# Performance work log

Hardware: AMD Instinct MI355X
Metric: run time of the kernel (lower is better)

## Reference

```python
import math
import jax, jax.numpy as jnp
import numpy as np

E = 1024
H = 16
DH = E // H
R = 8
ALPHA = 16
LORA_S = ALPHA / R

def build_slopes(h):
    start = 2 ** (-2 ** (-(math.log2(h) - 3)))
    return jnp.asarray([start * start ** i for i in range(h)], dtype=jnp.float32)

def setup_inputs() -> dict:
    key = jax.random.key(0)
    ks = jax.random.split(key, 12)
    B, T = 2, 2048
    x = jax.random.normal(ks[0], (B, T, E), dtype=jnp.float32)
    # nn.Linear weights: [out_f, in_f]; LoRA A: [out_f, r], B: [r, in_f]
    def lin(k):
        return jax.random.normal(k, (E, E), dtype=jnp.float32) / math.sqrt(E)
    inp = {
        "x": x,
        "Wq": lin(ks[1]), "Aq": jax.random.normal(ks[2], (E, R)) * 0.01, "Bq": jax.random.normal(ks[3], (R, E)) * 0.01,
        "Wk": lin(ks[4]), "Ak": jax.random.normal(ks[5], (E, R)) * 0.01, "Bk": jax.random.normal(ks[6], (R, E)) * 0.01,
        "Wv": lin(ks[7]), "Av": jax.random.normal(ks[8], (E, R)) * 0.01, "Bv": jax.random.normal(ks[9], (R, E)) * 0.01,
        "Wp": lin(ks[10]),
    }
    return inp

def _lora(x, W, A, Bm):
    # x @ W.T + (x @ B.T) @ A.T * s
    return x @ W.T + ((x @ Bm.T) @ A.T) * LORA_S

def reference(x, Wq, Aq, Bq, Wk, Ak, Bk, Wv, Av, Bv, Wp):
    B, T, _ = x.shape
    slopes = build_slopes(H)  # [H]
    q = _lora(x, Wq, Aq, Bq).reshape(B, T, H, DH).transpose(0, 2, 1, 3)  # [B,H,T,dh]
    k = _lora(x, Wk, Ak, Bk).reshape(B, T, H, DH).transpose(0, 2, 1, 3)
    v = _lora(x, Wv, Av, Bv).reshape(B, T, H, DH).transpose(0, 2, 1, 3)
    s = jnp.einsum("bhqd,bhkd->bhqk", q, k) / math.sqrt(DH)
    i = jnp.arange(T, dtype=jnp.float32)[:, None]
    j = jnp.arange(T, dtype=jnp.float32)[None, :]
    alibi = slopes[:, None, None] * (i - j)  # [H,T,T]
    mask = jnp.triu(jnp.full((T, T), -jnp.inf, dtype=jnp.float32), 1)
    s = s + alibi[None] + mask
    p = jax.nn.softmax(s, axis=-1)
    o = jnp.einsum("bhqk,bhkd->bhqd", p, v).transpose(0, 2, 1, 3).reshape(B, T, E)
    return o @ Wp.T
```

## Files before the change

### kernel.cpp

```cpp
#include <hip/hip_runtime.h>

typedef unsigned short u16;
typedef unsigned int   u32;
typedef __bf16 bf16_t;
typedef bf16_t bf16x8 __attribute__((ext_vector_type(8)));
typedef bf16_t bf16x2v __attribute__((ext_vector_type(2)));
typedef float  f32x4  __attribute__((ext_vector_type(4)));

#define E_DIM 1024
#define T_DIM 2048
#define H_NUM 16
#define DH 64
#define BT 4096
#define Y_LD 2048

__device__ __forceinline__ u16 f2bf(float f) {
  u32 u = __builtin_bit_cast(u32, f);
  u32 r = (u + 0x7fffu + ((u >> 16) & 1u)) >> 16;
  return (u16)r;
}
__device__ __forceinline__ float bf2f(u16 v) {
  u32 u = ((u32)v) << 16;
  return __builtin_bit_cast(float, u);
}

__device__ __forceinline__ float fexp2(float x) {
#if __has_builtin(__builtin_amdgcn_exp2f)
  return __builtin_amdgcn_exp2f(x);
#else
  return exp2f(x);
#endif
}

__device__ __forceinline__ int swz(int r, int c) {
  return r * 64 + (c ^ ((r & 7) << 3));
}

__device__ __forceinline__ void store_val(float* p, float v) { *p = v; }
__device__ __forceinline__ void store_val(u16* p, float v)   { *p = f2bf(v); }

typedef __attribute__((address_space(3))) unsigned int as3_u32;
typedef const __attribute__((address_space(1))) unsigned int as1_u32;

__device__ __forceinline__ void async16(const u16* g, u16* l) {
  __builtin_amdgcn_global_load_lds((as1_u32*)g, (as3_u32*)l, 16, 0, 0);
}

__device__ __forceinline__ void waitvm0_barrier() {
  asm volatile("s_waitcnt vmcnt(0)" ::: "memory");
  __builtin_amdgcn_s_barrier();
  __builtin_amdgcn_sched_barrier(0);
}

__device__ __forceinline__ u32 pack2(float a, float b) {
  bf16x2v v;
  v[0] = (bf16_t)a;
  v[1] = (bf16_t)b;
  return __builtin_bit_cast(u32, v);
}

__device__ __forceinline__ void plswap(u32& a, u32& b) {
#if __has_builtin(__builtin_amdgcn_permlane32_swap)
  typedef u32 u32x2 __attribute__((ext_vector_type(2)));
  u32x2 r = __builtin_amdgcn_permlane32_swap(a, b, false, false);
  a = r[0];
  b = r[1];
#else
  asm volatile("v_permlane32_swap_b32 %0, %1" : "+v"(a), "+v"(b));
#endif
}

__device__ __forceinline__ void redist_pair(u32 A, u32 B, bool odd, u32& wj, u32& wj2) {
  plswap(A, B);
  u32 sA = __builtin_amdgcn_ds_swizzle(A, 0x401F);
  u32 sB = __builtin_amdgcn_ds_swizzle(B, 0x401F);
  wj  = odd ? sB : A;
  wj2 = odd ? B : sA;
}

__global__ __launch_bounds__(256) void k_prep(
    const float* __restrict__ x,
    const float* __restrict__ W0, const float* __restrict__ A0, const float* __restrict__ B0,
    const float* __restrict__ W1, const float* __restrict__ A1, const float* __restrict__ B1,
    const float* __restrict__ W2, const float* __restrict__ A2, const float* __restrict__ B2,
    const float* __restrict__ Wp,
    u16* __restrict__ xb, u16* __restrict__ Weff, u16* __restrict__ Wpb, float s0) {
  const int blk = blockIdx.x;
  const int tid = threadIdx.x;
  if (blk < 4096) {
    int i = (blk * 256 + tid) * 4;
    float4 v = *reinterpret_cast<const float4*>(x + i);
    u32 lo = (u32)f2bf(v.x) | ((u32)f2bf(v.y) << 16);
    u32 hi = (u32)f2bf(v.z) | ((u32)f2bf(v.w) << 16);
    *reinterpret_cast<uint2*>(xb + i) = make_uint2(lo, hi);
  } else if (blk < 7168) {
    int e4 = (blk - 4096) * 256 + tid;
    int m = e4 >> 18;
    int e = (e4 & 262143) * 4;
    const float* W  = (m == 0) ? W0 : (m == 1) ? W1 : W2;
    const float* A  = (m == 0) ? A0 : (m == 1) ? A1 : A2;
    const float* Bm = (m == 0) ? B0 : (m == 1) ? B1 : B2;
    const float sc  = (m == 0) ? s0 : 1.0f;
    int o = e >> 10, i = e & 1023;
    float4 wv = *reinterpret_cast<const float4*>(W + e);
    float acc[4] = {wv.x, wv.y, wv.z, wv.w};
#pragma unroll
    for (int r = 0; r < 8; ++r) {
      float a2 = 2.0f * A[o * 8 + r];
      float4 bv = *reinterpret_cast<const float4*>(Bm + r * 1024 + i);
      acc[0] += a2 * bv.x; acc[1] += a2 * bv.y; acc[2] += a2 * bv.z; acc[3] += a2 * bv.w;
    }
    u32 lo = (u32)f2bf(acc[0] * sc) | ((u32)f2bf(acc[1] * sc) << 16);
    u32 hi = (u32)f2bf(acc[2] * sc) | ((u32)f2bf(acc[3] * sc) << 16);
    *reinterpret_cast<uint2*>(Weff + (size_t)m * 1048576 + e) = make_uint2(lo, hi);
  } else {
    int i = ((blk - 7168) * 256 + tid) * 4;
    float4 v = *reinterpret_cast<const float4*>(Wp + i);
    u32 lo = (u32)f2bf(v.x) | ((u32)f2bf(v.y) << 16);
    u32 hi = (u32)f2bf(v.z) | ((u32)f2bf(v.w) << 16);
    *reinterpret_cast<uint2*>(Wpb + i) = make_uint2(lo, hi);
  }
}

template <typename OUT_T, bool QKV>
__global__ __launch_bounds__(512) void k_gemm2(
    const u16* __restrict__ A, const u16* __restrict__ B,
    OUT_T* __restrict__ C, u16* __restrict__ Vt, int K, int ldc) {
  __shared__ __align__(16) u16 As[2][8192];
  __shared__ __align__(16) u16 Bs[2][8192];
  const int tid  = threadIdx.x;
  const int lane = tid & 63;
  const int wave = tid >> 6;
  const int wr = wave >> 2;
  const int wc = wave & 3;
  const int m0 = blockIdx.y * 128;
  const int n0 = blockIdx.x * 128;
  const int lr = lane & 15;
  const int lk = (lane >> 4) * 8;
  const bool vmode = QKV && (n0 >= 2048);

  f32x4 acc[4][2] = {};

  auto stageg = [&](int bufi, int t) {
#pragma unroll
    for (int p = 0; p < 2; ++p) {
      const int off = (p * 8 + wave) * 512;
      const int e = off + lane * 8;
      const int r = e >> 6, c = e & 63;
      const int cs = c ^ ((r & 7) << 3);
      async16(&A[(size_t)(m0 + r) * K + t * 64 + cs], &As[bufi][off]);
      async16(&B[(size_t)(n0 + r) * K + t * 64 + cs], &Bs[bufi][off]);
    }
  };

  const int nt = K >> 6;
  stageg(0, 0);
  waitvm0_barrier();
  int buf = 0;

  for (int t = 0; t < nt; ++t) {
    if (t + 1 < nt) stageg(buf ^ 1, t + 1);
    __builtin_amdgcn_s_setprio(1);
#pragma unroll
    for (int kk = 0; kk < 2; ++kk) {
      bf16x8 af[4], bfr[2];
#pragma unroll
      for (int mi = 0; mi < 4; ++mi)
        af[mi] = *reinterpret_cast<const bf16x8*>(&As[buf][swz(wr * 64 + mi * 16 + lr, kk * 32 + lk)]);
#pragma unroll
      for (int ni = 0; ni < 2; ++ni)
        bfr[ni] = *reinterpret_cast<const bf16x8*>(&Bs[buf][swz(wc * 32 + ni * 16 + lr, kk * 32 + lk)]);
      if (vmode) {
#pragma unroll
        for (int mi = 0; mi < 4; ++mi)
#pragma unroll
          for (int ni = 0; ni < 2; ++ni)
            acc[mi][ni] = __builtin_amdgcn_mfma_f32_16x16x32_bf16(bfr[ni], af[mi], acc[mi][ni], 0, 0, 0);
      } else {
#pragma unroll
        for (int mi = 0; mi < 4; ++mi)
#pragma unroll
          for (int ni = 0; ni < 2; ++ni)
            acc[mi][ni] = __builtin_amdgcn_mfma_f32_16x16x32_bf16(af[mi], bfr[ni], acc[mi][ni], 0, 0, 0);
      }
    }
    __builtin_amdgcn_s_setprio(0);
    waitvm0_barrier();
    buf ^= 1;
  }

  const int rg = (lane >> 4) * 4;
  if (vmode) {
#pragma unroll
    for (int mi = 0; mi < 4; ++mi)
#pragma unroll
      for (int ni = 0; ni < 2; ++ni)
#pragma unroll
        for (int q = 0; q < 4; ++q) {
          int o = n0 - 2048 + wc * 32 + ni * 16 + rg + q;
          int h = o >> 6, d = o & 63;
          int rowm = m0 + wr * 64 + mi * 16 + lr;
          int b = rowm >> 11, t = rowm & 2047;
          Vt[(size_t)(((b << 4) + h) * 64 + d) * 2048 + t] = f2bf(acc[mi][ni][q]);
        }
  } else {
#pragma unroll
    for (int mi = 0; mi < 4; ++mi)
#pragma unroll
      for (int ni = 0; ni < 2; ++ni)
#pragma unroll
        for (int q = 0; q < 4; ++q) {
          int row = m0 + wr * 64 + mi * 16 + rg + q;
          int col = n0 + wc * 32 + ni * 16 + lr;
          store_val(&C[(size_t)row * ldc + col], acc[mi][ni][q]);
        }
  }
}

__global__ __launch_bounds__(256) void k_attn8(
    const u16* __restrict__ Y, const u16* __restrict__ Vt, u16* __restrict__ Og,
    u16* __restrict__ Oa, u16* __restrict__ Ob,
    float* __restrict__ la, float* __restrict__ lb) {
  __shared__ __align__(16) u16 Ks[2][4096];
  __shared__ __align__(16) u16 Vs[2][4096];

  const int tid = threadIdx.x;
  const int lane = tid & 63;
  const int wave = tid >> 6;
  const int lr = lane & 15;
  const int lg = lane >> 4;
  const int lk = lg * 8;
  const bool odd = (lane & 16) != 0;

  const int orig = blockIdx.x;
  const int bh = orig & 31;
  const int c  = orig >> 5;
  const int qt = (c < 16) ? (16 + c) : (47 - c);
  const int ks = (c >= 16 && c < 32) ? 16 : 0;
  int ke       = (c < 16) ? 15 : qt;
  const int b = bh >> 4, h = bh & 15;

  const float LOG2E = 1.4426950408889634f;
  const float slope2 = exp2f(-0.5f * (float)(h + 1)) * LOG2E;

  const int Th = min(32, (int)(150.0f / slope2) / 64 + 1);
  ke = min(ke, Th - 1);

  if (ks > ke) {
    const int base = b * 1024 + (qt * 64 - 1024);
#pragma unroll
    for (int p = 0; p < 2; ++p) {
      int idx = p * 256 + tid;
      int rr = idx >> 3, cc8 = (idx & 7) * 8;
      uint4 z = {0, 0, 0, 0};
      *reinterpret_cast<uint4*>(&Ob[(size_t)(base + rr) * E_DIM + h * DH + cc8]) = z;
    }
    if (tid < 64) lb[bh * 1024 + (qt * 64 - 1024) + tid] = 0.f;
    return;
  }

  const u16* Kb = Y + (size_t)b * T_DIM * Y_LD + 1024 + h * DH;
  const u16* Vb = Vt + (size_t)bh * DH * T_DIM;

  bf16x8 qf[2];
  {
    const int qrow = qt * 64 + wave * 16 + lr;
#pragma unroll
    for (int kk = 0; kk < 2; ++kk)
      qf[kk] = *reinterpret_cast<const bf16x8*>(
          &Y[(size_t)(b * T_DIM + qrow) * Y_LD + h * DH + kk * 32 + lk]);
  }

  float nkb[16];
#pragma unroll
  for (int ni = 0; ni < 4; ++ni)
#pragma unroll
    for (int r = 0; r < 4; ++r)
      nkb[ni * 4 + r] = -slope2 * (float)(ni * 16 + lg * 4 + r) - 12.0f;

  bf16x8 ones;
#pragma unroll
  for (int jj = 0; jj < 8; ++jj) ones[jj] = (bf16_t)1.0f;

  f32x4 oacc[4] = {};
  f32x4 lacc = {};

  auto stage = [&](int bufi, int kt) {
    const int kv0 = kt * 64;
#pragma unroll
    for (int q = 0; q < 2; ++q) {
      const int off = (q * 4 + wave) * 512;
      const int e = off + lane * 8;
      const int r = e >> 6, cc = e & 63;
      const int cs = cc ^ ((r & 7) << 3);
      async16(Kb + (size_t)(kv0 + r) * Y_LD + cs, &Ks[bufi][off]);
      async16(Vb + (size_t)r * T_DIM + kv0 + cs, &Vs[bufi][off]);
    }
  };

  auto step = [&](int kt, int buf, bool DIAG) {
    f32x4 s[4] = {};
    __builtin_amdgcn_s_setprio(1);
#pragma unroll
    for (int kk = 0; kk < 2; ++kk)
#pragma unroll
      for (int ni = 0; ni < 4; ++ni) {
        bf16x8 kf = *reinterpret_cast<const bf16x8*>(&Ks[buf][swz(ni * 16 + lr, kk * 32 + lk)]);
        s[ni] = __builtin_amdgcn_mfma_f32_16x16x32_bf16(kf, qf[kk], s[ni], 0, 0, 0);
      }
    __builtin_amdgcn_s_setprio(0);
    const float ck = -slope2 * (float)(kt * 64);
    u32 pk[4][2];
#pragma unroll
    for (int ni = 0; ni < 4; ++ni) {
      float p[4];
#pragma unroll
      for (int r = 0; r < 4; ++r) {
        float sc = s[ni][r] + nkb[ni * 4 + r] + ck;
        if (DIAG && (ni * 16 + lg * 4 + r) > (wave * 16 + lr)) sc = -INFINITY;
        p[r] = fexp2(sc);
      }
      pk[ni][0] = pack2(p[0], p[1]);
      pk[ni][1] = pack2(p[2], p[3]);
    }
    uint4 PW[2];
#pragma unroll
    for (int kk = 0; kk < 2; ++kk) {
      redist_pair(pk[2 * kk][0], pk[2 * kk + 1][0], odd, PW[kk].x, PW[kk].z);
      redist_pair(pk[2 * kk][1], pk[2 * kk + 1][1], odd, PW[kk].y, PW[kk].w);
    }
    __builtin_amdgcn_s_setprio(1);
#pragma unroll
    for (int kk = 0; kk < 2; ++kk) {
      bf16x8 ph = __builtin_bit_cast(bf16x8, PW[kk]);
      lacc = __builtin_amdgcn_mfma_f32_16x16x32_bf16(ph, ones, lacc, 0, 0, 0);
#pragma unroll
      for (int f = 0; f < 4; ++f) {
        bf16x8 vf = *reinterpret_cast<const bf16x8*>(&Vs[buf][swz(f * 16 + lr, kk * 32 + lk)]);
        oacc[f] = __builtin_amdgcn_mfma_f32_16x16x32_bf16(ph, vf, oacc[f], 0, 0, 0);
      }
    }
    __builtin_amdgcn_s_setprio(0);
  };

  stage(0, ks);
  waitvm0_barrier();
  int buf = 0;
  for (int kt = ks; kt <= ke; ++kt) {
    if (kt < ke) stage(buf ^ 1, kt + 1);
    step(kt, buf, kt == qt);
    waitvm0_barrier();
    buf ^= 1;
  }

  if (c >= 32) {
    float linv[4];
#pragma unroll
    for (int r = 0; r < 4; ++r) linv[r] = 1.0f / lacc[r];
#pragma unroll
    for (int f = 0; f < 4; ++f)
#pragma unroll
      for (int r = 0; r < 4; ++r) {
        int q = qt * 64 + wave * 16 + lg * 4 + r;
        Og[(size_t)(b * T_DIM + q) * E_DIM + h * DH + f * 16 + lr] =
            f2bf(oacc[f][r] * linv[r]);
      }
  } else {
    u16* Op   = (c < 16) ? Oa : Ob;
    float* lp = (c < 16) ? la : lb;
#pragma unroll
    for (int f = 0; f < 4; ++f)
#pragma unroll
      for (int r = 0; r < 4; ++r) {
        int q = qt * 64 + wave * 16 + lg * 4 + r;
        Op[(size_t)(b * 1024 + (q - 1024)) * E_DIM + h * DH + f * 16 + lr] =
            f2bf(oacc[f][r]);
      }
    if (lr == 0) {
#pragma unroll
      for (int r = 0; r < 4; ++r) {
        int q = qt * 64 + wave * 16 + lg * 4 + r;
        lp[bh * 1024 + (q - 1024)] = lacc[r];
      }
    }
  }
}

__global__ __launch_bounds__(256) void k_merge(
    const u16* __restrict__ Oa, const u16* __restrict__ Ob,
    const float* __restrict__ la, const float* __restrict__ lb,
    u16* __restrict__ Og) {
  int idx = blockIdx.x * 256 + threadIdx.x;
  int row = idx >> 8;
  int cg  = (idx & 255) * 4;
  int b = row >> 10, tl = row & 1023;
  int h = cg >> 6;
  size_t po = (size_t)row * E_DIM + cg;
  uint2 ua = *reinterpret_cast<const uint2*>(Oa + po);
  uint2 ub = *reinterpret_cast<const uint2*>(Ob + po);
  float l = la[((b << 4) + h) * 1024 + tl] + lb[((b << 4) + h) * 1024 + tl];
  float inv = 1.0f / l;
  const u16* pa = reinterpret_cast<const u16*>(&ua);
  const u16* pb = reinterpret_cast<const u16*>(&ub);
  u16 o[4];
#pragma unroll
  for (int j = 0; j < 4; ++j)
    o[j] = f2bf((bf2f(pa[j]) + bf2f(pb[j])) * inv);
  *reinterpret_cast<uint2*>(Og + (size_t)(b * T_DIM + 1024 + tl) * E_DIM + cg) =
      *reinterpret_cast<const uint2*>(o);
}

extern "C" void kernel_launch(void* const* d_in, const int* in_sizes, int n_in,
                              void* d_out, int out_size, void* d_ws, size_t ws_size,
                              hipStream_t stream) {
  const float* x  = (const float*)d_in[0];
  const float* Wq = (const float*)d_in[1];
  const float* Aq = (const float*)d_in[2];
  const float* Bq = (const float*)d_in[3];
  const float* Wk = (const float*)d_in[4];
  const float* Ak = (const float*)d_in[5];
  const float* Bk = (const float*)d_in[6];
  const float* Wv = (const float*)d_in[7];
  const float* Av = (const float*)d_in[8];
  const float* Bv = (const float*)d_in[9];
  const float* Wp = (const float*)d_in[10];
  float* out = (float*)d_out;

  char* ws = (char*)d_ws;
  const size_t MB = 1048576;
  u16* xb   = (u16*)(ws);
  u16* Oa   = (u16*)(ws);
  u16* Ob   = (u16*)(ws + 4 * MB);
  u16* Weff = (u16*)(ws + 8 * MB);
  float* la = (float*)(ws + 8 * MB);
  float* lb = (float*)(ws + 8 * MB + 131072);
  u16* Yq   = (u16*)(ws + 14 * MB);
  u16* VtB  = (u16*)(ws + 30 * MB);
  u16* Wpb  = (u16*)(ws + 38 * MB);
  u16* Og   = (u16*)(ws + 40 * MB);

  const float ISQ2 = 0.125f * 1.4426950408889634f;

  k_prep<<<8192, 256, 0, stream>>>(x, Wq, Aq, Bq, Wk, Ak, Bk, Wv, Av, Bv, Wp,
                                   xb, Weff, Wpb, ISQ2);
  {
    dim3 grid(24, 32);
    k_gemm2<u16, true><<<grid, 512, 0, stream>>>(xb, Weff, Yq, VtB, E_DIM, Y_LD);
  }
  k_attn8<<<1536, 256, 0, stream>>>(Yq, VtB, Og, Oa, Ob, la, lb);
  k_merge<<<2048, 256, 0, stream>>>(Oa, Ob, la, lb, Og);
  {
    dim3 grid(8, 32);
    k_gemm2<float, false><<<grid, 512, 0, stream>>>(Og, Wpb, out, nullptr, E_DIM, E_DIM);
  }
}
```

Before: 107.6 us.

## Fuse split-attention merge into output projection and tighten ALiBi key cutoff

Removes the standalone merge kernel. The output projection GEMM now combines the two partial attention outputs, normalises them by the summed row sums and packs to bf16 while loading its A tile for the upper half of the sequence, which avoids a write and re-read of the merged activations. The attention grid is remapped so heads are scheduled from the highest index down with batch interleaved, for better load balance. The ALiBi distance cutoff is lowered from 150 to 64 log2 units so more far-away key tiles are skipped. The fused A-path uses synchronous global loads and register stores instead of async LDS copies, which may weaken load/compute overlap in the projection GEMM.

```diff
diff --git a/kernel.cpp b/kernel.cpp
--- a/kernel.cpp
+++ b/kernel.cpp
@@ -36,9 +36,6 @@
   return r * 64 + (c ^ ((r & 7) << 3));
 }
 
-__device__ __forceinline__ void store_val(float* p, float v) { *p = v; }
-__device__ __forceinline__ void store_val(u16* p, float v)   { *p = f2bf(v); }
-
 typedef __attribute__((address_space(3))) unsigned int as3_u32;
 typedef const __attribute__((address_space(1))) unsigned int as1_u32;
 
@@ -48,6 +45,12 @@
 
 __device__ __forceinline__ void waitvm0_barrier() {
   asm volatile("s_waitcnt vmcnt(0)" ::: "memory");
+  __builtin_amdgcn_s_barrier();
+  __builtin_amdgcn_sched_barrier(0);
+}
+
+__device__ __forceinline__ void waitall_barrier() {
+  asm volatile("s_waitcnt vmcnt(0) lgkmcnt(0)" ::: "memory");
   __builtin_amdgcn_s_barrier();
   __builtin_amdgcn_sched_barrier(0);
 }
@@ -122,10 +125,9 @@
   }
 }
 
-template <typename OUT_T, bool QKV>
 __global__ __launch_bounds__(512) void k_gemm2(
     const u16* __restrict__ A, const u16* __restrict__ B,
-    OUT_T* __restrict__ C, u16* __restrict__ Vt, int K, int ldc) {
+    u16* __restrict__ C, u16* __restrict__ Vt, int K, int ldc) {
   __shared__ __align__(16) u16 As[2][8192];
   __shared__ __align__(16) u16 Bs[2][8192];
   const int tid  = threadIdx.x;
@@ -137,7 +139,7 @@
   const int n0 = blockIdx.x * 128;
   const int lr = lane & 15;
   const int lk = (lane >> 4) * 8;
-  const bool vmode = QKV && (n0 >= 2048);
+  const bool vmode = (n0 >= 2048);
 
   f32x4 acc[4][2] = {};
 
@@ -212,9 +214,98 @@
         for (int q = 0; q < 4; ++q) {
           int row = m0 + wr * 64 + mi * 16 + rg + q;
           int col = n0 + wc * 32 + ni * 16 + lr;
-          store_val(&C[(size_t)row * ldc + col], acc[mi][ni][q]);
+          C[(size_t)row * ldc + col] = f2bf(acc[mi][ni][q]);
         }
   }
+}
+
+__global__ __launch_bounds__(512) void k_projm(
+    const u16* __restrict__ Og, const u16* __restrict__ Oa, const u16* __restrict__ Ob,
+    const float* __restrict__ la, const float* __restrict__ lb,
+    const u16* __restrict__ B, float* __restrict__ C) {
+  __shared__ __align__(16) u16 As[2][8192];
+  __shared__ __align__(16) u16 Bs[2][8192];
+  const int tid  = threadIdx.x;
+  const int lane = tid & 63;
+  const int wave = tid >> 6;
+  const int wr = wave >> 2, wc = wave & 3;
+  const int m0 = blockIdx.y * 128;
+  const int n0 = blockIdx.x * 128;
+  const int lr = lane & 15;
+  const int lk = (lane >> 4) * 8;
+  const bool upper = (m0 & 2047) >= 1024;
+  const int K = 1024;
+
+  f32x4 acc[4][2] = {};
+
+  auto stageg = [&](int bufi, int t) {
+#pragma unroll
+    for (int p = 0; p < 2; ++p) {
+      const int off = (p * 8 + wave) * 512;
+      const int e = off + lane * 8;
+      const int r = e >> 6, c = e & 63;
+      const int cs = c ^ ((r & 7) << 3);
+      async16(&B[(size_t)(n0 + r) * K + t * 64 + cs], &Bs[bufi][off]);
+      if (!upper) {
+        async16(&Og[(size_t)(m0 + r) * K + t * 64 + cs], &As[bufi][off]);
+      } else {
+        const int rowg = m0 + r;
+        const int bb = rowg >> 11, tl = (rowg & 2047) - 1024;
+        const int li = (bb * 16 + t) * 1024 + tl;
+        const float inv = 1.0f / (la[li] + lb[li]);
+        size_t po = (size_t)(bb * 1024 + tl) * 1024 + t * 64 + cs;
+        uint4 va = *reinterpret_cast<const uint4*>(Oa + po);
+        uint4 vb = *reinterpret_cast<const uint4*>(Ob + po);
+        const u16* pa = reinterpret_cast<const u16*>(&va);
+        const u16* pb = reinterpret_cast<const u16*>(&vb);
+        u16 o[8];
+#pragma unroll
+        for (int j = 0; j < 8; ++j) o[j] = f2bf((bf2f(pa[j]) + bf2f(pb[j])) * inv);
+        *reinterpret_cast<uint4*>(&As[bufi][off + lane * 8]) =
+            *reinterpret_cast<const uint4*>(o);
+      }
+    }
+  };
+
+  const int nt = K >> 6;
+  stageg(0, 0);
+  waitall_barrier();
+  int buf = 0;
+
+  for (int t = 0; t < nt; ++t) {
+    if (t + 1 < nt) stageg(buf ^ 1, t + 1);
+    __builtin_amdgcn_s_setprio(1);
+#pragma unroll
+    for (int kk = 0; kk < 2; ++kk) {
+      bf16x8 af[4], bfr[2];
+#pragma unroll
+      for (int mi = 0; mi < 4; ++mi)
+        af[mi] = *reinterpret_cast<const bf16x8*>(&As[buf][swz(wr * 64 + mi * 16 + lr, kk * 32 + lk)]);
+#pragma unroll
+      for (int ni = 0; ni < 2; ++ni)
+        bfr[ni] = *reinterpret_cast<const bf16x8*>(&Bs[buf][swz(wc * 32 + ni * 16 + lr, kk * 32 + lk)]);
+#pragma unroll
+      for (int mi = 0; mi < 4; ++mi)
+#pragma unroll
+        for (int ni = 0; ni < 2; ++ni)
+          acc[mi][ni] = __builtin_amdgcn_mfma_f32_16x16x32_bf16(af[mi], bfr[ni], acc[mi][ni], 0, 0, 0);
+    }
+    __builtin_amdgcn_s_setprio(0);
+    waitall_barrier();
+    buf ^= 1;
+  }
+
+  const int rg = (lane >> 4) * 4;
+#pragma unroll
+  for (int mi = 0; mi < 4; ++mi)
+#pragma unroll
+    for (int ni = 0; ni < 2; ++ni)
+#pragma unroll
+      for (int q = 0; q < 4; ++q) {
+        int row = m0 + wr * 64 + mi * 16 + rg + q;
+        int col = n0 + wc * 32 + ni * 16 + lr;
+        C[(size_t)row * 1024 + col] = acc[mi][ni][q];
+      }
 }
 
 __global__ __launch_bounds__(256) void k_attn8(
@@ -233,17 +324,19 @@
   const bool odd = (lane & 16) != 0;
 
   const int orig = blockIdx.x;
-  const int bh = orig & 31;
-  const int c  = orig >> 5;
+  const int h   = 15 - (orig / 96);
+  const int rem = orig % 96;
+  const int c   = rem >> 1;
+  const int b   = rem & 1;
+  const int bh  = b * 16 + h;
   const int qt = (c < 16) ? (16 + c) : (47 - c);
   const int ks = (c >= 16 && c < 32) ? 16 : 0;
   int ke       = (c < 16) ? 15 : qt;
-  const int b = bh >> 4, h = bh & 15;
 
   const float LOG2E = 1.4426950408889634f;
   const float slope2 = exp2f(-0.5f * (float)(h + 1)) * LOG2E;
 
-  const int Th = min(32, (int)(150.0f / slope2) / 64 + 1);
+  const int Th = min(32, (int)(64.0f / slope2) / 64 + 1);
   ke = min(ke, Th - 1);
 
   if (ks > ke) {
@@ -384,30 +477,6 @@
       }
     }
   }
-}
-
-__global__ __launch_bounds__(256) void k_merge(
-    const u16* __restrict__ Oa, const u16* __restrict__ Ob,
-    const float* __restrict__ la, const float* __restrict__ lb,
-    u16* __restrict__ Og) {
-  int idx = blockIdx.x * 256 + threadIdx.x;
-  int row = idx >> 8;
-  int cg  = (idx & 255) * 4;
-  int b = row >> 10, tl = row & 1023;
-  int h = cg >> 6;
-  size_t po = (size_t)row * E_DIM + cg;
-  uint2 ua = *reinterpret_cast<const uint2*>(Oa + po);
-  uint2 ub = *reinterpret_cast<const uint2*>(Ob + po);
-  float l = la[((b << 4) + h) * 1024 + tl] + lb[((b << 4) + h) * 1024 + tl];
-  float inv = 1.0f / l;
-  const u16* pa = reinterpret_cast<const u16*>(&ua);
-  const u16* pb = reinterpret_cast<const u16*>(&ub);
-  u16 o[4];
-#pragma unroll
-  for (int j = 0; j < 4; ++j)
-    o[j] = f2bf((bf2f(pa[j]) + bf2f(pb[j])) * inv);
-  *reinterpret_cast<uint2*>(Og + (size_t)(b * T_DIM + 1024 + tl) * E_DIM + cg) =
-      *reinterpret_cast<const uint2*>(o);
 }
 
 extern "C" void kernel_launch(void* const* d_in, const int* in_sizes, int n_in,
@@ -445,12 +514,11 @@
                                    xb, Weff, Wpb, ISQ2);
   {
     dim3 grid(24, 32);
-    k_gemm2<u16, true><<<grid, 512, 0, stream>>>(xb, Weff, Yq, VtB, E_DIM, Y_LD);
+    k_gemm2<<<grid, 512, 0, stream>>>(xb, Weff, Yq, VtB, E_DIM, Y_LD);
   }
   k_attn8<<<1536, 256, 0, stream>>>(Yq, VtB, Og, Oa, Ob, la, lb);
-  k_merge<<<2048, 256, 0, stream>>>(Oa, Ob, la, lb, Og);
   {
     dim3 grid(8, 32);
-    k_gemm2<float, false><<<grid, 512, 0, stream>>>(Og, Wpb, out, nullptr, E_DIM, E_DIM);
-  }
-}
+    k_projm<<<grid, 512, 0, stream>>>(Og, Oa, Ob, la, lb, Wpb, out);
+  }
+}
```

After: 107.7 us (median of 5 runs). Within noise of the previous version (+0.1%).
